# Kernel optimization log

Hardware: AMD Instinct MI355X
Metric: run time of the kernel (lower is better)

The kernel has to match this reference:

```python
import jax, jax.numpy as jnp
import numpy as np

N_NODES = 50000
N_EDGES = 1600000
DIM = 32
N_STEPS = 10   # torchdiffeq rk4 with step_size=0.1 over t in [0, 1]
H = 0.1


def setup_inputs() -> dict:
    key = jax.random.key(0)
    ks = jax.random.split(key, 10)
    x = jax.random.normal(ks[0], (N_NODES, DIM), dtype=jnp.float32)
    pos_edge_index = jax.random.randint(ks[1], (2, N_EDGES), 0, N_NODES, dtype=jnp.int64)
    neg_edge_index = jax.random.randint(ks[2], (2, N_EDGES), 0, N_NODES, dtype=jnp.int64)
    s = 1.0 / np.sqrt(DIM)
    W_pos = jax.random.normal(ks[3], (DIM, DIM), dtype=jnp.float32) * s
    b_pos = jnp.zeros((DIM,), dtype=jnp.float32)
    wt_pos = jax.random.normal(ks[4], (DIM,), dtype=jnp.float32)
    W_neg = jax.random.normal(ks[5], (DIM, DIM), dtype=jnp.float32) * s
    b_neg = jnp.zeros((DIM,), dtype=jnp.float32)
    wt_neg = jax.random.normal(ks[6], (DIM,), dtype=jnp.float32)
    return {"x": x, "pos_edge_index": pos_edge_index, "neg_edge_index": neg_edge_index,
            "W_pos": W_pos, "b_pos": b_pos, "wt_pos": wt_pos,
            "W_neg": W_neg, "b_neg": b_neg, "wt_neg": wt_neg}


def _gcn_ode(x0, edge_index, W, b, wt):
    # PyG GCNConv with self-loops + symmetric normalization, wrapped in
    # psi(t, x) = relu(GCN(x)) * sigmoid(t * wt), integrated with RK4.
    src, dst = edge_index[0], edge_index[1]
    n = x0.shape[0]
    deg = jnp.zeros((n,), dtype=x0.dtype).at[dst].add(1.0) + 1.0  # self-loop
    dis = jax.lax.rsqrt(deg)
    edge_norm = (dis[src] * dis[dst])[:, None]   # [E,1]
    self_norm = (dis * dis)[:, None]             # [N,1] = 1/deg

    def f(t, x):
        xw = x @ W                               # [N,D]
        agg = jax.ops.segment_sum(edge_norm * xw[src], dst, num_segments=n)
        agg = agg + self_norm * xw + b
        gate = jax.nn.sigmoid(t * wt)            # [D]
        return jax.nn.relu(agg) * gate

    def step(x, t):
        k1 = f(t, x)
        k2 = f(t + H / 2, x + (H / 2) * k1)
        k3 = f(t + H / 2, x + (H / 2) * k2)
        k4 = f(t + H, x + H * k3)
        return x + (H / 6) * (k1 + 2 * k2 + 2 * k3 + k4), None

    ts = jnp.arange(N_STEPS, dtype=x0.dtype) * H
    xT, _ = jax.lax.scan(step, x0, ts)
    return xT


def reference(x, pos_edge_index, neg_edge_index, W_pos, b_pos, wt_pos, W_neg, b_neg, wt_neg):
    z_pos = _gcn_ode(x, pos_edge_index, W_pos, b_pos, wt_pos)
    z_neg = _gcn_ode(x, neg_edge_index, W_neg, b_neg, wt_neg)
    return (z_pos, z_neg)
```

## Files before the change

### kernel.cpp

```cpp
#include <hip/hip_runtime.h>

#define NN 50000
#define NE 1600000
#define DIM 32
#define HS 0.1f
#define NBPS 782
#define NEB 6250
#define NEB4 1563
#define NNB 196
#define NSC 49

static inline int cdiv(int a, int b) { return (a + b - 1) / b; }

typedef unsigned short ushort_t;
typedef unsigned v4u __attribute__((ext_vector_type(4)));


__device__ __forceinline__ float4 bf4_to_f4(uint2 u) {
    float4 v;
    v.x = __uint_as_float(u.x << 16);
    v.y = __uint_as_float(u.x & 0xffff0000u);
    v.z = __uint_as_float(u.y << 16);
    v.w = __uint_as_float(u.y & 0xffff0000u);
    return v;
}
__device__ __forceinline__ unsigned pack_bf2(float a, float b) {
    unsigned ua = __float_as_uint(a);
    ua = (ua + 0x7fffu + ((ua >> 16) & 1u)) >> 16;
    unsigned ub = __float_as_uint(b);
    ub = (ub + 0x7fffu + ((ub >> 16) & 1u)) & 0xffff0000u;
    return ua | ub;
}
__device__ __forceinline__ uint4 pack_bf8(float4 a, float4 b) {
    return make_uint4(pack_bf2(a.x, a.y), pack_bf2(a.z, a.w),
                      pack_bf2(b.x, b.y), pack_bf2(b.z, b.w));
}


__global__ void k_zero2(int* __restrict__ p0, int* __restrict__ p1) {
    int b = blockIdx.x, sg = b & 1;
    int i = (b >> 1) * 256 + (int)threadIdx.x;
    int* p = sg ? p1 : p0;
    if (i < 2 * NN) p[i] = 0;
}

__global__ void k_zbins(int* __restrict__ bins) {
    bins[blockIdx.x * 256 + threadIdx.x] = 0;
}

__global__ void k_hist4(const int* __restrict__ dst, int* __restrict__ cnt) {
    int base = (blockIdx.x * 256 + (int)threadIdx.x) * 4;
    if (base < NE) {
        v4u d = *(const v4u*)(dst + base);
        atomicAdd(&cnt[d.x], 1);
        atomicAdd(&cnt[d.y], 1);
        atomicAdd(&cnt[d.z], 1);
        atomicAdd(&cnt[d.w], 1);
    }
}

__global__ void k_dhist2(const int* __restrict__ c0,
                         const int* __restrict__ c1, int* __restrict__ bins) {
    __shared__ int lb[256];
    int b = blockIdx.x, sg = b & 1;
    int t = threadIdx.x;
    lb[t] = 0;
    __syncthreads();
    int n = (b >> 1) * 256 + t;
    if (n < NN) {
        const int* cnt = sg ? c1 : c0;
        int d = cnt[n]; if (d > 255) d = 255;
        atomicAdd(&lb[d], 1);
    }
    __syncthreads();
    int v = lb[t];
    if (v) atomicAdd(&bins[sg * 256 + t], v);
}

__global__ void k_dscan(int* __restrict__ bins) {
    __shared__ int s[256];
    int sg = blockIdx.x, t = threadIdx.x;
    s[t] = bins[sg * 256 + (255 - t)];
    __syncthreads();
    for (int off = 1; off < 256; off <<= 1) {
        int a = (t >= off) ? s[t - off] : 0;
        __syncthreads();
        s[t] += a;
        __syncthreads();
    }
    int ex = (t == 0) ? 0 : s[t - 1];
    bins[sg * 256 + (255 - t)] = ex;
}

__global__ void k_dperm2(const int* __restrict__ c0,
                         const int* __restrict__ c1, int* __restrict__ bins,
                         int* __restrict__ perm0, int* __restrict__ perm1,
                         int* __restrict__ pos0, int* __restrict__ pos1,
                         float* __restrict__ q0, float* __restrict__ q1) {
    __shared__ int lb[256];
    int b = blockIdx.x, sg = b & 1;
    int t = threadIdx.x;
    lb[t] = 0;
    __syncthreads();
    int n = (b >> 1) * 256 + t;
    const int* cnt = sg ? c1 : c0;
    int d = 0, lr = 0;
    if (n < NN) {
        d = cnt[n]; if (d > 255) d = 255;
        lr = atomicAdd(&lb[d], 1);
    }
    __syncthreads();
    int v = lb[t];
    __syncthreads();
    int base = 0;
    if (v) base = atomicAdd(&bins[sg * 256 + t], v);
    lb[t] = base;
    __syncthreads();
    if (n < NN) {
        int p = lb[d] + lr;
        int* perm = sg ? perm1 : perm0;
        int* pos  = sg ? pos1 : pos0;
        float* dq = sg ? q1 : q0;
        perm[p] = n;
        pos[n] = p;
        dq[p] = rsqrtf((float)cnt[n] + 1.0f);
    }
}

__global__ __launch_bounds__(1024) void k_scanA2(const int* __restrict__ c0,
                                                 const int* __restrict__ c1,
                                                 const int* __restrict__ perm0,
                                                 const int* __restrict__ perm1,
                                                 int* __restrict__ r0,
                                                 int* __restrict__ r1,
                                                 int* __restrict__ p0,
                                                 int* __restrict__ p1) {
    int sg = blockIdx.x >= NSC;
    int bb = blockIdx.x - (sg ? NSC : 0);
    const int* cnt  = sg ? c1 : c0;
    const int* perm = sg ? perm1 : perm0;
    int* row_ptr    = sg ? r1 : r0;
    int* partials   = sg ? p1 : p0;
    __shared__ int s[1024];
    int t = threadIdx.x;
    int g = bb * 1024 + t;
    int v = (g < NN) ? ((cnt[perm[g]] + 7) & ~7) : 0;
    s[t] = v;
    __syncthreads();
    for (int off = 1; off < 1024; off <<= 1) {
        int add = (t >= off) ? s[t - off] : 0;
        __syncthreads();
        s[t] += add;
        __syncthreads();
    }
    if (g < NN) row_ptr[g + 1] = s[t];
    if (t == 1023) partials[bb] = s[t];
}

__global__ void k_scanB2(int* __restrict__ p0, int* __restrict__ p1) {
    int* partials = blockIdx.x ? p1 : p0;
    if (threadIdx.x == 0) {
        int run = 0;
        for (int i = 0; i < NSC; i++) { int v = partials[i]; partials[i] = run; run += v; }
    }
}

__global__ void k_scanC2(int* __restrict__ r0, int* __restrict__ r1,
                         const int* __restrict__ p0, const int* __restrict__ p1) {
    int b = blockIdx.x, sg = b & 1;
    int g = (b >> 1) * 256 + (int)threadIdx.x;
    int* row_ptr = sg ? r1 : r0;
    const int* partials = sg ? p1 : p0;
    if (g < NN) row_ptr[g + 1] += partials[g >> 10];
    if (g == 0) row_ptr[0] = 0;
}

__global__ void k_fillp(const int* __restrict__ src,
                        const int* __restrict__ dst,
                        const int* __restrict__ pos, const int* __restrict__ row_ptr,
                        int* __restrict__ fill, ushort_t* __restrict__ cw) {
    int i = blockIdx.x * blockDim.x + threadIdx.x;
    if (i < NE) {
        int ps = pos[src[i]], pd = pos[dst[i]];
        int slot = row_ptr[pd] + atomicAdd(&fill[pd], 1);
        cw[slot] = (ushort_t)ps;
    }
}

__global__ void k_pad2(const int* __restrict__ r0, const int* __restrict__ r1,
                       const int* __restrict__ c0, const int* __restrict__ c1,
                       const int* __restrict__ perm0, const int* __restrict__ perm1,
                       ushort_t* __restrict__ w0, ushort_t* __restrict__ w1) {
    int b = blockIdx.x, sg = b & 1;
    int p = (b >> 1) * 256 + (int)threadIdx.x;
    if (p < NN) {
        const int* row_ptr = sg ? r1 : r0;
        const int* cnt = sg ? c1 : c0;
        const int* perm = sg ? perm1 : perm0;
        ushort_t* cw = sg ? w1 : w0;
        int e = row_ptr[p] + cnt[perm[p]], e1 = row_ptr[p + 1];
        for (; e < e1; ++e) cw[e] = (ushort_t)NN;
    }
}

struct ZArgs { unsigned* p[6]; };
__global__ void k_zrow(ZArgs z) {
    int t = threadIdx.x;
    if (t < 96) z.p[t >> 4][(size_t)NN * 16 + (t & 15)] = 0u;
}

__global__ __launch_bounds__(256) void k_matmul(const float* __restrict__ src,
                                                const float* __restrict__ W,
                                                const int* __restrict__ cnt,
                                                const int* __restrict__ pos,
                                                uint2* __restrict__ xw,
                                                float* __restrict__ copy_out) {
    __shared__ float sW[DIM * DIM];
    __shared__ float sX[32 * 33];
    int t = threadIdx.x;
#pragma unroll
    for (int k = 0; k < 4; k++) { int i = k * 256 + t; sW[i] = W[i]; }
    size_t base = (size_t)blockIdx.x * 32 * DIM;
#pragma unroll
    for (int k = 0; k < 4; k++) {
        int i = k * 256 + t;
        size_t g = base + i;
        float v = 0.f;
        if (g < (size_t)NN * DIM) {
            v = src[g];
            copy_out[g] = v;
        }
        sX[(i >> 5) * 33 + (i & 31)] = v;
    }
    __syncthreads();
    int r = t >> 3, oct = t & 7;
    int row = blockIdx.x * 32 + r;
    if (row >= NN) return;
    float a0 = 0.f, a1 = 0.f, a2 = 0.f, a3 = 0.f;
    const float* xr = &sX[r * 33];
#pragma unroll
    for (int i = 0; i < DIM; i++) {
        float xv = xr[i];
        const float* wr = &sW[i * DIM + oct * 4];
        a0 = fmaf(xv, wr[0], a0);
        a1 = fmaf(xv, wr[1], a1);
        a2 = fmaf(xv, wr[2], a2);
        a3 = fmaf(xv, wr[3], a3);
    }
    float dn = rsqrtf((float)cnt[row] + 1.0f);
    a0 *= dn; a1 *= dn; a2 *= dn; a3 *= dn;
    xw[(size_t)pos[row] * 8 + oct] = make_uint2(pack_bf2(a0, a1), pack_bf2(a2, a3));
}


struct SignP {
    const int* row_ptr; const ushort_t* cw; const float* dis;
    const int* perm;
    const uint4* xw_in; uint4* xw_out; const uint4* xw_base;
    uint4* acc;
    float* x_cur;
    const float* W; const float* b; const float* wt;
    float* zout;
};
struct StageArgs { SignP s[2]; float t, stage_coef; int mode; };

#define EDGE_ADD(u)                                                     \
    {                                                                   \
        float4 vA = bf4_to_f4(make_uint2((u).x, (u).y));                \
        float4 vB = bf4_to_f4(make_uint2((u).z, (u).w));                \
        sum0.x += vA.x; sum0.y += vA.y; sum0.z += vA.z; sum0.w += vA.w; \
        sum1.x += vB.x; sum1.y += vB.y; sum1.z += vB.z; sum1.w += vB.w; \
    }

__global__ __launch_bounds__(256) void k_stage(StageArgs A) {
    int sg = blockIdx.x & 1;
    int blk = blockIdx.x >> 1;
    SignP P = A.s[sg];

    __shared__ float sW[DIM * DIM];
    __shared__ float sR[64 * 36];
    int tid = threadIdx.x;
    int mode = A.mode;
    if (mode != 5) {
#pragma unroll
        for (int k = 0; k < 4; k++) { int i = k * 256 + tid; sW[i] = P.W[i]; }
    }

    int c = tid & 3;
    int nl = tid >> 2;
    int n = blk * 64 + nl;
    bool active = n < NN;
    float dn = 0.f;
    float4 r40 = make_float4(0.f, 0.f, 0.f, 0.f);
    float4 r41 = make_float4(0.f, 0.f, 0.f, 0.f);
    float4 bs0 = make_float4(0.f, 0.f, 0.f, 0.f);
    float4 bs1 = make_float4(0.f, 0.f, 0.f, 0.f);

    if (active) {
        int e = P.row_ptr[n], e1 = P.row_ptr[n + 1];
        const uint4* xwq = P.xw_in + c;
        const uint4* cw4 = (const uint4*)P.cw;
        int q = e >> 3, qe = e1 >> 3;
        float4 sum0 = make_float4(0.f, 0.f, 0.f, 0.f);
        float4 sum1 = make_float4(0.f, 0.f, 0.f, 0.f);
        uint4 ra;
        if (q < qe) ra = cw4[q];
        while (q < qe) {
            unsigned s0 = ra.x & 0xffffu, s1 = ra.x >> 16;
            unsigned s2 = ra.y & 0xffffu, s3 = ra.y >> 16;
            unsigned s4 = ra.z & 0xffffu, s5 = ra.z >> 16;
            unsigned s6 = ra.w & 0xffffu, s7 = ra.w >> 16;
            uint4 u0 = xwq[(size_t)s0 * 4];
            uint4 u1 = xwq[(size_t)s1 * 4];
            uint4 u2 = xwq[(size_t)s2 * 4];
            uint4 u3 = xwq[(size_t)s3 * 4];
            uint4 u4 = xwq[(size_t)s4 * 4];
            uint4 u5 = xwq[(size_t)s5 * 4];
            uint4 u6 = xwq[(size_t)s6 * 4];
            uint4 u7 = xwq[(size_t)s7 * 4];
            int qn = q + 1;
            uint4 nx;
            if (qn < qe) nx = cw4[qn];
            EDGE_ADD(u0) EDGE_ADD(u1) EDGE_ADD(u2) EDGE_ADD(u3)
            EDGE_ADD(u4) EDGE_ADD(u5) EDGE_ADD(u6) EDGE_ADD(u7)
            if (qn < qe) ra = nx;
            q = qn;
        }
        dn = P.dis[n];
        uint4 un = xwq[(size_t)n * 4];
        float4 vn0 = bf4_to_f4(make_uint2(un.x, un.y));
        float4 vn1 = bf4_to_f4(make_uint2(un.z, un.w));
        float4 bb0 = *(const float4*)&P.b[c * 8];
        float4 bb1 = *(const float4*)&P.b[c * 8 + 4];
        sum0.x = fmaf(dn, sum0.x + vn0.x, bb0.x);
        sum0.y = fmaf(dn, sum0.y + vn0.y, bb0.y);
        sum0.z = fmaf(dn, sum0.z + vn0.z, bb0.z);
        sum0.w = fmaf(dn, sum0.w + vn0.w, bb0.w);
        sum1.x = fmaf(dn, sum1.x + vn1.x, bb1.x);
        sum1.y = fmaf(dn, sum1.y + vn1.y, bb1.y);
        sum1.z = fmaf(dn, sum1.z + vn1.z, bb1.z);
        sum1.w = fmaf(dn, sum1.w + vn1.w, bb1.w);
        float4 w40 = *(const float4*)&P.wt[c * 8];
        float4 w41 = *(const float4*)&P.wt[c * 8 + 4];
        float t = A.t;
        float4 kv0, kv1;
        kv0.x = fmaxf(sum0.x, 0.f) / (1.f + __expf(-t * w40.x));
        kv0.y = fmaxf(sum0.y, 0.f) / (1.f + __expf(-t * w40.y));
        kv0.z = fmaxf(sum0.z, 0.f) / (1.f + __expf(-t * w40.z));
        kv0.w = fmaxf(sum0.w, 0.f) / (1.f + __expf(-t * w40.w));
        kv1.x = fmaxf(sum1.x, 0.f) / (1.f + __expf(-t * w41.x));
        kv1.y = fmaxf(sum1.y, 0.f) / (1.f + __expf(-t * w41.y));
        kv1.z = fmaxf(sum1.z, 0.f) / (1.f + __expf(-t * w41.z));
        kv1.w = fmaxf(sum1.w, 0.f) / (1.f + __expf(-t * w41.w));

        uint4* accp = P.acc + (size_t)n * 4 + c;
        if (mode == 1) {
            *accp = pack_bf8(kv0, kv1);
            r40 = kv0; r41 = kv1;
            bs0 = vn0; bs1 = vn1;
        } else if (mode <= 3) {
            uint4 ao = *accp;
            float4 a0 = bf4_to_f4(make_uint2(ao.x, ao.y));
            float4 a1 = bf4_to_f4(make_uint2(ao.z, ao.w));
            a0.x = fmaf(2.f, kv0.x, a0.x); a0.y = fmaf(2.f, kv0.y, a0.y);
            a0.z = fmaf(2.f, kv0.z, a0.z); a0.w = fmaf(2.f, kv0.w, a0.w);
            a1.x = fmaf(2.f, kv1.x, a1.x); a1.y = fmaf(2.f, kv1.y, a1.y);
            a1.z = fmaf(2.f, kv1.z, a1.z); a1.w = fmaf(2.f, kv1.w, a1.w);
            *accp = pack_bf8(a0, a1);
            r40 = kv0; r41 = kv1;
            uint4 ub = P.xw_base[(size_t)n * 4 + c];
            bs0 = bf4_to_f4(make_uint2(ub.x, ub.y));
            bs1 = bf4_to_f4(make_uint2(ub.z, ub.w));
        } else {
            uint4 ao = *accp;
            float4 f0 = bf4_to_f4(make_uint2(ao.x, ao.y));
            float4 f1 = bf4_to_f4(make_uint2(ao.z, ao.w));
            f0.x += kv0.x; f0.y += kv0.y; f0.z += kv0.z; f0.w += kv0.w;
            f1.x += kv1.x; f1.y += kv1.y; f1.z += kv1.z; f1.w += kv1.w;
            int id = P.perm[n];
            size_t o = (size_t)id * DIM + c * 8;
            float4 xc0 = *(const float4*)&P.x_cur[o];
            float4 xc1 = *(const float4*)&P.x_cur[o + 4];
            float4 xn0, xn1;
            xn0.x = fmaf(HS / 6.f, f0.x, xc0.x); xn0.y = fmaf(HS / 6.f, f0.y, xc0.y);
            xn0.z = fmaf(HS / 6.f, f0.z, xc0.z); xn0.w = fmaf(HS / 6.f, f0.w, xc0.w);
            xn1.x = fmaf(HS / 6.f, f1.x, xc1.x); xn1.y = fmaf(HS / 6.f, f1.y, xc1.y);
            xn1.z = fmaf(HS / 6.f, f1.z, xc1.z); xn1.w = fmaf(HS / 6.f, f1.w, xc1.w);
            if (mode == 4) {
                *(float4*)&P.x_cur[o] = xn0;
                *(float4*)&P.x_cur[o + 4] = xn1;
                r40 = f0; r41 = f1;
                uint4 ub = P.xw_base[(size_t)n * 4 + c];
                bs0 = bf4_to_f4(make_uint2(ub.x, ub.y));
                bs1 = bf4_to_f4(make_uint2(ub.z, ub.w));
            } else {
                *(float4*)&P.zout[o] = xn0;
                *(float4*)&P.zout[o + 4] = xn1;
            }
        }
    }

    if (mode == 5) return;

    *(float4*)&sR[nl * 36 + c * 8] = r40;
    *(float4*)&sR[nl * 36 + c * 8 + 4] = r41;
    __syncthreads();
    if (active) {
        float4 y0 = make_float4(0.f, 0.f, 0.f, 0.f);
        float4 y1 = make_float4(0.f, 0.f, 0.f, 0.f);
        const float* row = &sR[nl * 36];
#pragma unroll
        for (int i = 0; i < DIM; i++) {
            float sv = row[i];
            float4 wA = *(const float4*)&sW[i * DIM + c * 8];
            float4 wB = *(const float4*)&sW[i * DIM + c * 8 + 4];
            y0.x = fmaf(sv, wA.x, y0.x); y0.y = fmaf(sv, wA.y, y0.y);
            y0.z = fmaf(sv, wA.z, y0.z); y0.w = fmaf(sv, wA.w, y0.w);
            y1.x = fmaf(sv, wB.x, y1.x); y1.y = fmaf(sv, wB.y, y1.y);
            y1.z = fmaf(sv, wB.z, y1.z); y1.w = fmaf(sv, wB.w, y1.w);
        }
        float sd = A.stage_coef * dn;
        y0.x = fmaf(sd, y0.x, bs0.x); y0.y = fmaf(sd, y0.y, bs0.y);
        y0.z = fmaf(sd, y0.z, bs0.z); y0.w = fmaf(sd, y0.w, bs0.w);
        y1.x = fmaf(sd, y1.x, bs1.x); y1.y = fmaf(sd, y1.y, bs1.y);
        y1.z = fmaf(sd, y1.z, bs1.z); y1.w = fmaf(sd, y1.w, bs1.w);
        P.xw_out[(size_t)n * 4 + c] = pack_bf8(y0, y1);
    }
}


extern "C" void kernel_launch(void* const* d_in, const int* in_sizes, int n_in,
                              void* d_out, int out_size, void* d_ws, size_t ws_size,
                              hipStream_t stream) {
    const float* x   = (const float*)d_in[0];
    const int* epos  = (const int*)d_in[1];
    const int* eneg  = (const int*)d_in[2];
    const float* Wp  = (const float*)d_in[3];
    const float* bp  = (const float*)d_in[4];
    const float* wtp = (const float*)d_in[5];
    const float* Wn  = (const float*)d_in[6];
    const float* bn  = (const float*)d_in[7];
    const float* wtn = (const float*)d_in[8];
    float* out = (float*)d_out;

    char* ws = (char*)d_ws;
    size_t off = 0;
    auto alloc = [&](size_t bytes) -> void* {
        void* p = ws + off;
        off += (bytes + 255) & ~(size_t)255;
        return p;
    };

    struct Sign {
        int *row_ptr, *cnt, *fill, *partials, *perm, *pos;
        float* dis;
        ushort_t* cw;
        float* x_cur;
        uint4* acc;
        uint4* xwbuf[3];
        const int *src, *dst;
        const float *W, *b, *wt;
        float* zout;
    } S[2];

    const size_t CWCAP = (size_t)NE + 8u * NN;
    int* dbins = (int*)alloc(2 * 256 * sizeof(int));

    for (int s = 0; s < 2; s++) {
        S[s].row_ptr  = (int*)alloc((NN + 1) * sizeof(int));
        int* cntfill  = (int*)alloc((size_t)2 * NN * sizeof(int));
        S[s].cnt  = cntfill;
        S[s].fill = cntfill + NN;
        S[s].partials = (int*)alloc(256);
        S[s].perm     = (int*)alloc(NN * sizeof(int));
        S[s].pos      = (int*)alloc(NN * sizeof(int));
        S[s].dis      = (float*)alloc(NN * sizeof(float));
        S[s].cw       = (ushort_t*)alloc(CWCAP * sizeof(ushort_t));
        S[s].x_cur    = (float*)alloc((size_t)NN * DIM * sizeof(float));
        S[s].acc      = (uint4*)alloc((size_t)NN * DIM * 2);
        S[s].xwbuf[0] = (uint4*)alloc((size_t)(NN + 1) * DIM * 2);
        S[s].xwbuf[1] = (uint4*)alloc((size_t)(NN + 1) * DIM * 2);
        S[s].xwbuf[2] = (uint4*)alloc((size_t)(NN + 1) * DIM * 2);
    }
    S[0].src = epos; S[0].dst = epos + NE; S[0].W = Wp; S[0].b = bp; S[0].wt = wtp;
    S[0].zout = out;
    S[1].src = eneg; S[1].dst = eneg + NE; S[1].W = Wn; S[1].b = bn; S[1].wt = wtn;
    S[1].zout = out + (size_t)NN * DIM;

    k_zero2<<<2 * cdiv(2 * NN, 256), 256, 0, stream>>>(S[0].cnt, S[1].cnt);
    k_zbins<<<2, 256, 0, stream>>>(dbins);
    for (int s = 0; s < 2; s++)
        k_hist4<<<NEB4, 256, 0, stream>>>(S[s].dst, S[s].cnt);
    k_dhist2<<<2 * NNB, 256, 0, stream>>>(S[0].cnt, S[1].cnt, dbins);
    k_dscan<<<2, 256, 0, stream>>>(dbins);
    k_dperm2<<<2 * NNB, 256, 0, stream>>>(S[0].cnt, S[1].cnt, dbins,
                                          S[0].perm, S[1].perm, S[0].pos, S[1].pos,
                                          S[0].dis, S[1].dis);
    k_scanA2<<<2 * NSC, 1024, 0, stream>>>(S[0].cnt, S[1].cnt, S[0].perm, S[1].perm,
                                           S[0].row_ptr, S[1].row_ptr,
                                           S[0].partials, S[1].partials);
    k_scanB2<<<2, 1, 0, stream>>>(S[0].partials, S[1].partials);
    k_scanC2<<<2 * NNB, 256, 0, stream>>>(S[0].row_ptr, S[1].row_ptr,
                                          S[0].partials, S[1].partials);
    for (int s = 0; s < 2; s++)
        k_fillp<<<NEB, 256, 0, stream>>>(S[s].src, S[s].dst, S[s].pos,
                                         S[s].row_ptr, S[s].fill, S[s].cw);
    k_pad2<<<2 * NNB, 256, 0, stream>>>(S[0].row_ptr, S[1].row_ptr,
                                        S[0].cnt, S[1].cnt,
                                        S[0].perm, S[1].perm, S[0].cw, S[1].cw);

    ZArgs Z;
    for (int s = 0; s < 2; s++)
        for (int k = 0; k < 3; k++) Z.p[s * 3 + k] = (unsigned*)S[s].xwbuf[k];
    k_zrow<<<1, 96, 0, stream>>>(Z);
    for (int s = 0; s < 2; s++)
        k_matmul<<<cdiv(NN, 32), 256, 0, stream>>>(x, S[s].W, S[s].cnt, S[s].pos,
                                                   (uint2*)S[s].xwbuf[0], S[s].x_cur);

    for (int st = 0; st < 10; st++) {
        float tb = HS * (float)st;
        struct Ph { float t, sc; int mode, in, out; } ph[4] = {
            { tb,             HS * 0.5f, 1,              0, 1 },
            { tb + HS * 0.5f, HS * 0.5f, 2,              1, 2 },
            { tb + HS * 0.5f, HS,        3,              2, 1 },
            { tb + HS,        HS / 6.f,  st == 9 ? 5 : 4, 1, 0 },
        };
        for (int p = 0; p < 4; p++) {
            StageArgs A;
            for (int s = 0; s < 2; s++) {
                A.s[s].row_ptr = S[s].row_ptr;
                A.s[s].cw      = S[s].cw;
                A.s[s].dis     = S[s].dis;
                A.s[s].perm    = S[s].perm;
                A.s[s].xw_in   = S[s].xwbuf[ph[p].in];
                A.s[s].xw_out  = S[s].xwbuf[ph[p].out];
                A.s[s].xw_base = S[s].xwbuf[0];
                A.s[s].acc     = S[s].acc;
                A.s[s].x_cur   = S[s].x_cur;
                A.s[s].W       = S[s].W;
                A.s[s].b       = S[s].b;
                A.s[s].wt      = S[s].wt;
                A.s[s].zout    = S[s].zout;
            }
            A.t = ph[p].t; A.stage_coef = ph[p].sc; A.mode = ph[p].mode;
            k_stage<<<2 * NBPS, 256, 0, stream>>>(A);
        }
    }
}
```

Before: 1.468 ms.

## Replace atomic CSR fill with two-level binned counting-sort scatter

Replaces the per-edge global-atomic CSR fill and padding kernels with a two-pass bucketed sort. Edges are first counted and staged into 196 destination bins through shared memory, and the per-block offsets come from a scan. Each bin is then placed into a shared-memory window and written out coalesced, with padding fused into the same pass. The aim is to remove scattered global atomics and random 2-byte writes, at the cost of more kernel launches and an extra staging buffer per graph.

Measured after the change: 1.382 ms. -5.8%, faster.

```diff
diff --git a/kernel.cpp b/kernel.cpp
--- a/kernel.cpp
+++ b/kernel.cpp
@@ -5,10 +5,13 @@
 #define DIM 32
 #define HS 0.1f
 #define NBPS 782
-#define NEB 6250
 #define NEB4 1563
 #define NNB 196
 #define NSC 49
+#define SBIN 256
+#define NBIN 196
+#define AB 391
+#define WCAP 22528
 
 static inline int cdiv(int a, int b) { return (a + b - 1) / b; }
 
@@ -41,7 +44,7 @@
     int b = blockIdx.x, sg = b & 1;
     int i = (b >> 1) * 256 + (int)threadIdx.x;
     int* p = sg ? p1 : p0;
-    if (i < 2 * NN) p[i] = 0;
+    if (i < NN) p[i] = 0;
 }
 
 __global__ void k_zbins(int* __restrict__ bins) {
@@ -175,31 +178,188 @@
     if (g == 0) row_ptr[0] = 0;
 }
 
-__global__ void k_fillp(const int* __restrict__ src,
-                        const int* __restrict__ dst,
-                        const int* __restrict__ pos, const int* __restrict__ row_ptr,
-                        int* __restrict__ fill, ushort_t* __restrict__ cw) {
-    int i = blockIdx.x * blockDim.x + threadIdx.x;
-    if (i < NE) {
-        int ps = pos[src[i]], pd = pos[dst[i]];
-        int slot = row_ptr[pd] + atomicAdd(&fill[pd], 1);
-        cw[slot] = (ushort_t)ps;
-    }
-}
-
-__global__ void k_pad2(const int* __restrict__ r0, const int* __restrict__ r1,
-                       const int* __restrict__ c0, const int* __restrict__ c1,
-                       const int* __restrict__ perm0, const int* __restrict__ perm1,
-                       ushort_t* __restrict__ w0, ushort_t* __restrict__ w1) {
-    int b = blockIdx.x, sg = b & 1;
-    int p = (b >> 1) * 256 + (int)threadIdx.x;
-    if (p < NN) {
-        const int* row_ptr = sg ? r1 : r0;
-        const int* cnt = sg ? c1 : c0;
-        const int* perm = sg ? perm1 : perm0;
-        ushort_t* cw = sg ? w1 : w0;
-        int e = row_ptr[p] + cnt[perm[p]], e1 = row_ptr[p + 1];
-        for (; e < e1; ++e) cw[e] = (ushort_t)NN;
+
+__global__ __launch_bounds__(512) void k_countA(const int* __restrict__ d0,
+                        const int* __restrict__ d1,
+                        const int* __restrict__ pos0, const int* __restrict__ pos1,
+                        int* __restrict__ gc0, int* __restrict__ gc1) {
+    __shared__ int lc[NBIN];
+    int b = blockIdx.x, sg = b & 1, blk = b >> 1;
+    int t = threadIdx.x;
+    if (t < NBIN) lc[t] = 0;
+    __syncthreads();
+    const int* dst = sg ? d1 : d0;
+    const int* pos = sg ? pos1 : pos0;
+#pragma unroll
+    for (int i = 0; i < 8; i++) {
+        int e = blk * 4096 + i * 512 + t;
+        if (e < NE) atomicAdd(&lc[pos[dst[e]] >> 8], 1);
+    }
+    __syncthreads();
+    int* gc = sg ? gc1 : gc0;
+    if (t < NBIN) gc[blk * NBIN + t] = lc[t];
+}
+
+__global__ __launch_bounds__(512) void k_scanM1(int* __restrict__ gc0,
+                                                int* __restrict__ gc1,
+                                                int* __restrict__ bint) {
+    __shared__ int s[512];
+    int b = blockIdx.x, sg = b & 1, bin = b >> 1;
+    int* gc = sg ? gc1 : gc0;
+    int t = threadIdx.x;
+    int v = (t < AB) ? gc[t * NBIN + bin] : 0;
+    s[t] = v;
+    __syncthreads();
+    for (int off = 1; off < 512; off <<= 1) {
+        int a = (t >= off) ? s[t - off] : 0;
+        __syncthreads();
+        s[t] += a;
+        __syncthreads();
+    }
+    if (t < AB) gc[t * NBIN + bin] = s[t] - v;
+    if (t == AB - 1) bint[sg * NBIN + bin] = s[t];
+}
+
+__global__ __launch_bounds__(256) void k_scanM2(const int* __restrict__ bint,
+                                                int* __restrict__ binbase) {
+    __shared__ int s[256];
+    int t = threadIdx.x;
+    for (int sg = 0; sg < 2; sg++) {
+        int v = (t < NBIN) ? bint[sg * NBIN + t] : 0;
+        s[t] = v;
+        __syncthreads();
+        for (int off = 1; off < 256; off <<= 1) {
+            int a = (t >= off) ? s[t - off] : 0;
+            __syncthreads();
+            s[t] += a;
+            __syncthreads();
+        }
+        if (t < NBIN) binbase[sg * NBIN + t] = s[t] - v;
+        __syncthreads();
+    }
+}
+
+__global__ __launch_bounds__(512) void k_scatA(const int* __restrict__ s0s,
+                        const int* __restrict__ s0d,
+                        const int* __restrict__ s1s, const int* __restrict__ s1d,
+                        const int* __restrict__ pos0, const int* __restrict__ pos1,
+                        const int* __restrict__ gc0, const int* __restrict__ gc1,
+                        const int* __restrict__ binbase,
+                        unsigned* __restrict__ gst0, unsigned* __restrict__ gst1) {
+    __shared__ int lc[NBIN];
+    __shared__ int lst[NBIN];
+    __shared__ int gch[NBIN];
+    __shared__ unsigned stag[4096];
+    __shared__ ushort_t bos[4096];
+    int b = blockIdx.x, sg = b & 1, blk = b >> 1;
+    int t = threadIdx.x;
+    if (t < NBIN) lc[t] = 0;
+    __syncthreads();
+    const int* src = sg ? s1s : s0s;
+    const int* dst = sg ? s1d : s0d;
+    const int* pos = sg ? pos1 : pos0;
+    const int* gc  = sg ? gc1 : gc0;
+    unsigned er[8]; int ebin[8]; int erk[8];
+#pragma unroll
+    for (int i = 0; i < 8; i++) {
+        int e = blk * 4096 + i * 512 + t;
+        ebin[i] = -1;
+        if (e < NE) {
+            int pd = pos[dst[e]];
+            int ps = pos[src[e]];
+            int bin = pd >> 8;
+            ebin[i] = bin;
+            er[i] = ((unsigned)ps << 8) | (unsigned)(pd & 255);
+            erk[i] = atomicAdd(&lc[bin], 1);
+        }
+    }
+    __syncthreads();
+    if (t < NBIN) lst[t] = lc[t];
+    __syncthreads();
+    for (int off = 1; off < NBIN; off <<= 1) {
+        int a = (t >= off && t < NBIN) ? lst[t - off] : 0;
+        __syncthreads();
+        if (t < NBIN) lst[t] += a;
+        __syncthreads();
+    }
+    if (t < NBIN) {
+        lst[t] -= lc[t];
+        gch[t] = binbase[sg * NBIN + t] + gc[blk * NBIN + t];
+    }
+    __syncthreads();
+#pragma unroll
+    for (int i = 0; i < 8; i++) {
+        if (ebin[i] >= 0) {
+            int slot = lst[ebin[i]] + erk[i];
+            stag[slot] = er[i];
+            bos[slot] = (ushort_t)ebin[i];
+        }
+    }
+    __syncthreads();
+    unsigned* gst = sg ? gst1 : gst0;
+    int tot = (blk * 4096 + 4096 <= NE) ? 4096 : (NE - blk * 4096);
+#pragma unroll
+    for (int i = 0; i < 8; i++) {
+        int slot = i * 512 + t;
+        if (slot < tot) {
+            int bin = bos[slot];
+            gst[gch[bin] + (slot - lst[bin])] = stag[slot];
+        }
+    }
+}
+
+__global__ __launch_bounds__(512) void k_scatB(const int* __restrict__ r0,
+                        const int* __restrict__ r1,
+                        const unsigned* __restrict__ gst0,
+                        const unsigned* __restrict__ gst1,
+                        const int* __restrict__ bint, const int* __restrict__ binbase,
+                        ushort_t* __restrict__ w0, ushort_t* __restrict__ w1) {
+    __shared__ uint4 winq[WCAP / 8];
+    __shared__ int lrp[SBIN + 1];
+    __shared__ int lfill[SBIN];
+    ushort_t* win = (ushort_t*)winq;
+    int b = blockIdx.x, sg = b & 1, bin = b >> 1;
+    int t = threadIdx.x;
+    const int* rp = sg ? r1 : r0;
+    const unsigned* gst = sg ? gst1 : gst0;
+    ushort_t* cw = sg ? w1 : w0;
+    int p0 = bin * SBIN;
+    int nn = NN - p0; if (nn > SBIN) nn = SBIN;
+    if (t <= nn) lrp[t] = rp[p0 + t];
+    if (t < nn) lfill[t] = 0;
+    __syncthreads();
+    int wb = lrp[0];
+    int wl = lrp[nn] - wb;
+    int cnt = bint[sg * NBIN + bin];
+    int base = binbase[sg * NBIN + bin];
+    if (wl <= WCAP) {
+        for (int i = t; i < cnt; i += 512) {
+            unsigned e = gst[base + i];
+            int pdl = e & 255u;
+            int ofs = atomicAdd(&lfill[pdl], 1);
+            win[lrp[pdl] - wb + ofs] = (ushort_t)(e >> 8);
+        }
+        __syncthreads();
+        for (int ln = t; ln < nn; ln += 512) {
+            int e0 = lrp[ln] - wb + lfill[ln], e1 = lrp[ln + 1] - wb;
+            for (int j = e0; j < e1; j++) win[j] = (ushort_t)NN;
+        }
+        __syncthreads();
+        uint4* dst4 = (uint4*)(cw + wb);
+        int nq = wl >> 3;
+        for (int i = t; i < nq; i += 512) dst4[i] = winq[i];
+    } else {
+        for (int i = t; i < cnt; i += 512) {
+            unsigned e = gst[base + i];
+            int pdl = e & 255u;
+            int ofs = atomicAdd(&lfill[pdl], 1);
+            cw[lrp[pdl] + ofs] = (ushort_t)(e >> 8);
+        }
+        __syncthreads();
+        for (int ln = t; ln < nn; ln += 512) {
+            int e0 = lrp[ln] + lfill[ln], e1 = lrp[ln + 1];
+            for (int j = e0; j < e1; j++) cw[j] = (ushort_t)NN;
+        }
     }
 }
 
@@ -452,7 +612,8 @@
     };
 
     struct Sign {
-        int *row_ptr, *cnt, *fill, *partials, *perm, *pos;
+        int *row_ptr, *cnt, *partials, *perm, *pos, *gcnt;
+        unsigned* gstage;
         float* dis;
         ushort_t* cw;
         float* x_cur;
@@ -464,16 +625,18 @@
     } S[2];
 
     const size_t CWCAP = (size_t)NE + 8u * NN;
-    int* dbins = (int*)alloc(2 * 256 * sizeof(int));
+    int* dbins   = (int*)alloc(2 * 256 * sizeof(int));
+    int* bint    = (int*)alloc(2 * NBIN * sizeof(int));
+    int* binbase = (int*)alloc(2 * NBIN * sizeof(int));
 
     for (int s = 0; s < 2; s++) {
         S[s].row_ptr  = (int*)alloc((NN + 1) * sizeof(int));
-        int* cntfill  = (int*)alloc((size_t)2 * NN * sizeof(int));
-        S[s].cnt  = cntfill;
-        S[s].fill = cntfill + NN;
+        S[s].cnt      = (int*)alloc(NN * sizeof(int));
         S[s].partials = (int*)alloc(256);
         S[s].perm     = (int*)alloc(NN * sizeof(int));
         S[s].pos      = (int*)alloc(NN * sizeof(int));
+        S[s].gcnt     = (int*)alloc((size_t)AB * NBIN * sizeof(int));
+        S[s].gstage   = (unsigned*)alloc((size_t)NE * sizeof(unsigned));
         S[s].dis      = (float*)alloc(NN * sizeof(float));
         S[s].cw       = (ushort_t*)alloc(CWCAP * sizeof(ushort_t));
         S[s].x_cur    = (float*)alloc((size_t)NN * DIM * sizeof(float));
@@ -487,7 +650,7 @@
     S[1].src = eneg; S[1].dst = eneg + NE; S[1].W = Wn; S[1].b = bn; S[1].wt = wtn;
     S[1].zout = out + (size_t)NN * DIM;
 
-    k_zero2<<<2 * cdiv(2 * NN, 256), 256, 0, stream>>>(S[0].cnt, S[1].cnt);
+    k_zero2<<<2 * NNB, 256, 0, stream>>>(S[0].cnt, S[1].cnt);
     k_zbins<<<2, 256, 0, stream>>>(dbins);
     for (int s = 0; s < 2; s++)
         k_hist4<<<NEB4, 256, 0, stream>>>(S[s].dst, S[s].cnt);
@@ -502,12 +665,16 @@
     k_scanB2<<<2, 1, 0, stream>>>(S[0].partials, S[1].partials);
     k_scanC2<<<2 * NNB, 256, 0, stream>>>(S[0].row_ptr, S[1].row_ptr,
                                           S[0].partials, S[1].partials);
-    for (int s = 0; s < 2; s++)
-        k_fillp<<<NEB, 256, 0, stream>>>(S[s].src, S[s].dst, S[s].pos,
-                                         S[s].row_ptr, S[s].fill, S[s].cw);
-    k_pad2<<<2 * NNB, 256, 0, stream>>>(S[0].row_ptr, S[1].row_ptr,
-                                        S[0].cnt, S[1].cnt,
-                                        S[0].perm, S[1].perm, S[0].cw, S[1].cw);
+    k_countA<<<2 * AB, 512, 0, stream>>>(S[0].dst, S[1].dst, S[0].pos, S[1].pos,
+                                         S[0].gcnt, S[1].gcnt);
+    k_scanM1<<<2 * NBIN, 512, 0, stream>>>(S[0].gcnt, S[1].gcnt, bint);
+    k_scanM2<<<1, 256, 0, stream>>>(bint, binbase);
+    k_scatA<<<2 * AB, 512, 0, stream>>>(S[0].src, S[0].dst, S[1].src, S[1].dst,
+                                        S[0].pos, S[1].pos, S[0].gcnt, S[1].gcnt,
+                                        binbase, S[0].gstage, S[1].gstage);
+    k_scatB<<<2 * NBIN, 512, 0, stream>>>(S[0].row_ptr, S[1].row_ptr,
+                                          S[0].gstage, S[1].gstage,
+                                          bint, binbase, S[0].cw, S[1].cw);
 
     ZArgs Z;
     for (int s = 0; s < 2; s++)
```
